# Kernel tuning notes

Hardware: AMD Instinct MI355X
Metric: run time of the kernel (lower is better)

The kernel has to match this reference:

```python
import jax, jax.numpy as jnp
import numpy as np

NOISE_SCALE = 0.1
NOISE_RATIO = 0.3
TEMPERATURE = 1.0
ADAPTIVE_FACTOR = 1.0
MAX_NOISE = 1.0


def setup_inputs() -> dict:
    key = jax.random.key(0)
    k1, k2, k3, k4 = jax.random.split(key, 4)
    B, D, C = 4096, 4096, 1000
    x = jax.random.normal(k1, (B, D), dtype=jnp.float32)
    model_output = jax.random.normal(k2, (B, C), dtype=jnp.float32)
    rand_u = jax.random.uniform(k3, (B, D), dtype=jnp.float32)
    noise_std = jax.random.normal(k4, (B, D), dtype=jnp.float32)
    return {"x": x, "model_output": model_output, "rand_u": rand_u, "noise_std": noise_std}


def reference(x, model_output, rand_u, noise_std):
    # per-sample confidence = max softmax prob of temperature-scaled logits
    probs = jax.nn.softmax(model_output / TEMPERATURE, axis=1)          # [B, C]
    confidence = jnp.max(probs, axis=1)                                  # [B]
    # adaptive per-sample noise scale, clamped at MAX_NOISE
    scales = jnp.minimum(NOISE_SCALE * (1.0 + ADAPTIVE_FACTOR * confidence), MAX_NOISE)  # [B]
    noise = noise_std * scales[:, None]                                  # [B, D]
    mask = rand_u < NOISE_RATIO                                          # [B, D] bool
    return x + jnp.where(mask, noise, jnp.zeros((), dtype=x.dtype))
```

## Files before the change

kernel.cpp:

```cpp
#include <hip/hip_runtime.h>
#include <math.h>

#define B_DIM 4096
#define D_DIM 4096
#define C_DIM 1000

typedef float v4f __attribute__((ext_vector_type(4)));

__global__ __launch_bounds__(256) void compute_scales(
    const float* __restrict__ mo,
    float* __restrict__ scales)
{
    const int row  = blockIdx.x * 4 + (threadIdx.x >> 6);
    const int lane = threadIdx.x & 63;
    const v4f* mo4 = (const v4f*)(mo + (size_t)row * C_DIM);

    const v4f NEG = {-INFINITY, -INFINITY, -INFINITY, -INFINITY};
    const v4f a = mo4[lane];
    const v4f b = mo4[lane + 64];
    const v4f c = mo4[lane + 128];
    const v4f d = (lane < 58) ? mo4[lane + 192] : NEG;

    float lm = fmaxf(fmaxf(fmaxf(a.x, a.y), fmaxf(a.z, a.w)),
                     fmaxf(fmaxf(b.x, b.y), fmaxf(b.z, b.w)));
    lm = fmaxf(lm, fmaxf(fmaxf(c.x, c.y), fmaxf(c.z, c.w)));
    lm = fmaxf(lm, fmaxf(fmaxf(d.x, d.y), fmaxf(d.z, d.w)));
    #pragma unroll
    for (int off = 32; off > 0; off >>= 1)
        lm = fmaxf(lm, __shfl_xor(lm, off, 64));

    float ls = __expf(a.x - lm) + __expf(a.y - lm) + __expf(a.z - lm) + __expf(a.w - lm)
             + __expf(b.x - lm) + __expf(b.y - lm) + __expf(b.z - lm) + __expf(b.w - lm)
             + __expf(c.x - lm) + __expf(c.y - lm) + __expf(c.z - lm) + __expf(c.w - lm)
             + __expf(d.x - lm) + __expf(d.y - lm) + __expf(d.z - lm) + __expf(d.w - lm);
    #pragma unroll
    for (int off = 32; off > 0; off >>= 1)
        ls += __shfl_xor(ls, off, 64);

    if (lane == 0)
        scales[row] = fminf(0.1f * (1.0f + 1.0f / ls), 1.0f);
}

__global__ __launch_bounds__(256) void stream_add(
    const float* __restrict__ x,
    const float* __restrict__ rand_u,
    const float* __restrict__ noise_std,
    const float* __restrict__ scales,
    float* __restrict__ out)
{
    const int b = blockIdx.x;
    const int t = threadIdx.x;
    const float scale = scales[b];

    const size_t rowf4 = (size_t)b * (D_DIM / 4);
    const v4f* x4 = (const v4f*)x         + rowf4;
    const v4f* r4 = (const v4f*)rand_u    + rowf4;
    const v4f* n4 = (const v4f*)noise_std + rowf4;
    v4f*       o4 = (v4f*)out             + rowf4;

    #pragma unroll
    for (int k = 0; k < 4; ++k) {
        const int idx = k * 256 + t;
        const v4f xv = __builtin_nontemporal_load(x4 + idx);
        const v4f rv = __builtin_nontemporal_load(r4 + idx);
        const v4f nv = __builtin_nontemporal_load(n4 + idx);
        v4f ov;
        ov.x = xv.x + (rv.x < 0.3f ? nv.x * scale : 0.0f);
        ov.y = xv.y + (rv.y < 0.3f ? nv.y * scale : 0.0f);
        ov.z = xv.z + (rv.z < 0.3f ? nv.z * scale : 0.0f);
        ov.w = xv.w + (rv.w < 0.3f ? nv.w * scale : 0.0f);
        o4[idx] = ov;
    }
}

extern "C" void kernel_launch(void* const* d_in, const int* in_sizes, int n_in,
                              void* d_out, int out_size, void* d_ws, size_t ws_size,
                              hipStream_t stream) {
    const float* x            = (const float*)d_in[0];
    const float* model_output = (const float*)d_in[1];
    const float* rand_u       = (const float*)d_in[2];
    const float* noise_std    = (const float*)d_in[3];
    float* out    = (float*)d_out;
    float* scales = (float*)d_ws;

    compute_scales<<<B_DIM / 4, 256, 0, stream>>>(model_output, scales);
    stream_add<<<B_DIM, 256, 0, stream>>>(x, rand_u, noise_std, scales, out);
}
```

Measured before the change: 211.5 us.

## Fuse softmax-confidence scale computation into the streaming add kernel

Merges the two kernels into one: each block reads its row of logits (redundantly across its 4 wavefronts), computes the max-softmax scale with wave reductions, and applies the masked noise add. All streaming loads are issued before the reduction so the memory latency overlaps the softmax math. This removes a kernel launch, the scales workspace round trip and the dependency between launches. In exchange, every wavefront recomputes the same row reduction and register pressure rises from holding 12 vectors per thread.

```diff
diff --git a/kernel.cpp b/kernel.cpp
--- a/kernel.cpp
+++ b/kernel.cpp
@@ -7,50 +7,24 @@
 
 typedef float v4f __attribute__((ext_vector_type(4)));
 
-__global__ __launch_bounds__(256) void compute_scales(
+__global__ __launch_bounds__(256) void adaptive_noise_onepass(
+    const float* __restrict__ x,
     const float* __restrict__ mo,
-    float* __restrict__ scales)
-{
-    const int row  = blockIdx.x * 4 + (threadIdx.x >> 6);
-    const int lane = threadIdx.x & 63;
-    const v4f* mo4 = (const v4f*)(mo + (size_t)row * C_DIM);
-
-    const v4f NEG = {-INFINITY, -INFINITY, -INFINITY, -INFINITY};
-    const v4f a = mo4[lane];
-    const v4f b = mo4[lane + 64];
-    const v4f c = mo4[lane + 128];
-    const v4f d = (lane < 58) ? mo4[lane + 192] : NEG;
-
-    float lm = fmaxf(fmaxf(fmaxf(a.x, a.y), fmaxf(a.z, a.w)),
-                     fmaxf(fmaxf(b.x, b.y), fmaxf(b.z, b.w)));
-    lm = fmaxf(lm, fmaxf(fmaxf(c.x, c.y), fmaxf(c.z, c.w)));
-    lm = fmaxf(lm, fmaxf(fmaxf(d.x, d.y), fmaxf(d.z, d.w)));
-    #pragma unroll
-    for (int off = 32; off > 0; off >>= 1)
-        lm = fmaxf(lm, __shfl_xor(lm, off, 64));
-
-    float ls = __expf(a.x - lm) + __expf(a.y - lm) + __expf(a.z - lm) + __expf(a.w - lm)
-             + __expf(b.x - lm) + __expf(b.y - lm) + __expf(b.z - lm) + __expf(b.w - lm)
-             + __expf(c.x - lm) + __expf(c.y - lm) + __expf(c.z - lm) + __expf(c.w - lm)
-             + __expf(d.x - lm) + __expf(d.y - lm) + __expf(d.z - lm) + __expf(d.w - lm);
-    #pragma unroll
-    for (int off = 32; off > 0; off >>= 1)
-        ls += __shfl_xor(ls, off, 64);
-
-    if (lane == 0)
-        scales[row] = fminf(0.1f * (1.0f + 1.0f / ls), 1.0f);
-}
-
-__global__ __launch_bounds__(256) void stream_add(
-    const float* __restrict__ x,
     const float* __restrict__ rand_u,
     const float* __restrict__ noise_std,
-    const float* __restrict__ scales,
     float* __restrict__ out)
 {
-    const int b = blockIdx.x;
-    const int t = threadIdx.x;
-    const float scale = scales[b];
+    const int b    = blockIdx.x;
+    const int t    = threadIdx.x;
+    const int lane = t & 63;
+
+    const v4f* mo4 = (const v4f*)(mo + (size_t)b * C_DIM);
+    const v4f NEG = {-INFINITY, -INFINITY, -INFINITY, -INFINITY};
+    const v4f la = mo4[lane];
+    const v4f lb = mo4[lane + 64];
+    const v4f lc = mo4[lane + 128];
+    v4f ld = NEG;
+    if (lane < 58) ld = mo4[lane + 192];
 
     const size_t rowf4 = (size_t)b * (D_DIM / 4);
     const v4f* x4 = (const v4f*)x         + rowf4;
@@ -58,17 +32,41 @@
     const v4f* n4 = (const v4f*)noise_std + rowf4;
     v4f*       o4 = (v4f*)out             + rowf4;
 
+    v4f xv[4], rv[4], nv[4];
     #pragma unroll
     for (int k = 0; k < 4; ++k) {
         const int idx = k * 256 + t;
-        const v4f xv = __builtin_nontemporal_load(x4 + idx);
-        const v4f rv = __builtin_nontemporal_load(r4 + idx);
-        const v4f nv = __builtin_nontemporal_load(n4 + idx);
+        xv[k] = __builtin_nontemporal_load(x4 + idx);
+        rv[k] = __builtin_nontemporal_load(r4 + idx);
+        nv[k] = __builtin_nontemporal_load(n4 + idx);
+    }
+
+    float lm = fmaxf(fmaxf(fmaxf(la.x, la.y), fmaxf(la.z, la.w)),
+                     fmaxf(fmaxf(lb.x, lb.y), fmaxf(lb.z, lb.w)));
+    lm = fmaxf(lm, fmaxf(fmaxf(lc.x, lc.y), fmaxf(lc.z, lc.w)));
+    lm = fmaxf(lm, fmaxf(fmaxf(ld.x, ld.y), fmaxf(ld.z, ld.w)));
+    #pragma unroll
+    for (int off = 32; off > 0; off >>= 1)
+        lm = fmaxf(lm, __shfl_xor(lm, off, 64));
+
+    float ls = __expf(la.x - lm) + __expf(la.y - lm) + __expf(la.z - lm) + __expf(la.w - lm)
+             + __expf(lb.x - lm) + __expf(lb.y - lm) + __expf(lb.z - lm) + __expf(lb.w - lm)
+             + __expf(lc.x - lm) + __expf(lc.y - lm) + __expf(lc.z - lm) + __expf(lc.w - lm)
+             + __expf(ld.x - lm) + __expf(ld.y - lm) + __expf(ld.z - lm) + __expf(ld.w - lm);
+    #pragma unroll
+    for (int off = 32; off > 0; off >>= 1)
+        ls += __shfl_xor(ls, off, 64);
+
+    const float scale = fminf(0.1f * (1.0f + 1.0f / ls), 1.0f);
+
+    #pragma unroll
+    for (int k = 0; k < 4; ++k) {
+        const int idx = k * 256 + t;
         v4f ov;
-        ov.x = xv.x + (rv.x < 0.3f ? nv.x * scale : 0.0f);
-        ov.y = xv.y + (rv.y < 0.3f ? nv.y * scale : 0.0f);
-        ov.z = xv.z + (rv.z < 0.3f ? nv.z * scale : 0.0f);
-        ov.w = xv.w + (rv.w < 0.3f ? nv.w * scale : 0.0f);
+        ov.x = xv[k].x + (rv[k].x < 0.3f ? nv[k].x * scale : 0.0f);
+        ov.y = xv[k].y + (rv[k].y < 0.3f ? nv[k].y * scale : 0.0f);
+        ov.z = xv[k].z + (rv[k].z < 0.3f ? nv[k].z * scale : 0.0f);
+        ov.w = xv[k].w + (rv[k].w < 0.3f ? nv[k].w * scale : 0.0f);
         o4[idx] = ov;
     }
 }
@@ -80,9 +78,8 @@
     const float* model_output = (const float*)d_in[1];
     const float* rand_u       = (const float*)d_in[2];
     const float* noise_std    = (const float*)d_in[3];
-    float* out    = (float*)d_out;
-    float* scales = (float*)d_ws;
+    float* out = (float*)d_out;
 
-    compute_scales<<<B_DIM / 4, 256, 0, stream>>>(model_output, scales);
-    stream_add<<<B_DIM, 256, 0, stream>>>(x, rand_u, noise_std, scales, out);
+    adaptive_noise_onepass<<<B_DIM, 256, 0, stream>>>(
+        x, model_output, rand_u, noise_std, out);
 }
```

Result: no change. 209.4 us (-1.0%).
